# Optimization experiments

Hardware: AMD Instinct MI355X
Metric: run time of the kernel (lower is better)

Reference implementation:

```python
import jax, jax.numpy as jnp
import numpy as np

N_NODES = 50000
N_GRAPHS = 512
HID = 128
IN = 128
SLOPE = 0.2  # LeakyReLU negative slope (PyG default)


def _gatv2(x, src, dst, Wl, bl, Wr, br, att, bias, n):
    # PyG GATv2Conv, 1 head: xl used for source/messages, xr for targets
    xl = x @ Wl + bl          # [N, H]
    xr = x @ Wr + br          # [N, H]
    # per-edge score: att . LeakyReLU(xl[j] + xr[i])
    e = jax.nn.leaky_relu(xl[src] + xr[dst], SLOPE) @ att  # [E]
    # softmax grouped by destination node (self loops guarantee nonempty groups)
    m = jax.ops.segment_max(e, dst, num_segments=n)
    p = jnp.exp(e - m[dst])
    s = jax.ops.segment_sum(p, dst, num_segments=n)
    alpha = p / s[dst]                                      # [E]
    out = jax.ops.segment_sum(alpha[:, None] * xl[src], dst, num_segments=n)
    return out + bias


def setup_inputs() -> dict:
    key = jax.random.key(0)
    ks = jax.random.split(key, 24)
    x = jax.random.normal(ks[0], (N_NODES, IN), jnp.float32)
    edge_index = jax.random.randint(ks[1], (2, 1600000), 0, N_NODES, jnp.int64)
    batch = jnp.sort(jax.random.randint(ks[2], (N_NODES,), 0, N_GRAPHS, jnp.int64))

    def lin(k, fi, fo):
        k1, k2 = jax.random.split(k)
        sc = 1.0 / np.sqrt(fi)
        return (jax.random.uniform(k1, (fi, fo), jnp.float32, -sc, sc),
                jax.random.uniform(k2, (fo,), jnp.float32, -sc, sc))

    d = {"x": x, "edge_index": edge_index, "batch": batch}
    dims = [(IN, HID), (HID, HID), (HID, HID)]
    for i, (fi, fo) in enumerate(dims, 1):
        Wl, bl = lin(ks[3 * i], fi, fo)
        Wr, br = lin(ks[3 * i + 1], fi, fo)
        d[f"Wl{i}"], d[f"bl{i}"] = Wl, bl
        d[f"Wr{i}"], d[f"br{i}"] = Wr, br
        d[f"att{i}"] = jax.random.normal(ks[3 * i + 2], (fo,), jnp.float32) / np.sqrt(fo)
        d[f"bias{i}"] = jnp.zeros((fo,), jnp.float32)
    d["W4"], d["b4"] = lin(ks[15], HID, 128)
    d["W5"], d["b5"] = lin(ks[16], 128, 64)
    d["W6"], d["b6"] = lin(ks[17], 64, 2)
    return d


def reference(x, edge_index, batch,
              Wl1, bl1, Wr1, br1, att1, bias1,
              Wl2, bl2, Wr2, br2, att2, bias2,
              Wl3, bl3, Wr3, br3, att3, bias3,
              W4, b4, W5, b5, W6, b6):
    n = x.shape[0]
    loop = jnp.arange(n, dtype=edge_index.dtype)
    src = jnp.concatenate([edge_index[0], loop])  # add_self_loops=True
    dst = jnp.concatenate([edge_index[1], loop])

    h = jax.nn.relu(_gatv2(x, src, dst, Wl1, bl1, Wr1, br1, att1, bias1, n))
    h = jax.nn.relu(_gatv2(h, src, dst, Wl2, bl2, Wr2, br2, att2, bias2, n))
    h = _gatv2(h, src, dst, Wl3, bl3, Wr3, br3, att3, bias3, n)

    # global_mean_pool over graph ids
    sums = jax.ops.segment_sum(h, batch, num_segments=N_GRAPHS)
    cnts = jax.ops.segment_sum(jnp.ones((n,), h.dtype), batch, num_segments=N_GRAPHS)
    g = sums / jnp.maximum(cnts, 1.0)[:, None]

    # dropout is identity in eval mode; MLP head
    g = jax.nn.sigmoid(g @ W4 + b4)
    g = jax.nn.sigmoid(g @ W5 + b5)
    return g @ W6 + b6
```

## Files before the change

### kernel.cpp

```cpp
#include <hip/hip_runtime.h>
#include <hip/hip_bf16.h>
#include <math.h>

#define BK_SHIFT 7
#define BK_NODES 128

typedef _Float16 h2 __attribute__((ext_vector_type(2)));

__device__ __forceinline__ h2 u2h(unsigned u){ return __builtin_bit_cast(h2, u); }

__device__ __forceinline__ int dev_lower_bound(const int* __restrict__ a, int n, int v){
  int lo = 0, hi = n;
  while (lo < hi){ int mid = (lo + hi) >> 1; if (a[mid] < v) lo = mid + 1; else hi = mid; }
  return lo;
}

__global__ __launch_bounds__(256) void p1_bucket_count(const int* __restrict__ edst,
    int* __restrict__ bktTotal, int nE, int K){
  __shared__ int cnt[512];
  for (int k = threadIdx.x; k < K; k += 256) cnt[k] = 0;
  __syncthreads();
  int i = (blockIdx.x * 256 + threadIdx.x) * 8;
  if (i + 7 < nE){
    int4 a = *(const int4*)(edst + i);
    int4 b = *(const int4*)(edst + i + 4);
    atomicAdd(&cnt[a.x >> BK_SHIFT], 1); atomicAdd(&cnt[a.y >> BK_SHIFT], 1);
    atomicAdd(&cnt[a.z >> BK_SHIFT], 1); atomicAdd(&cnt[a.w >> BK_SHIFT], 1);
    atomicAdd(&cnt[b.x >> BK_SHIFT], 1); atomicAdd(&cnt[b.y >> BK_SHIFT], 1);
    atomicAdd(&cnt[b.z >> BK_SHIFT], 1); atomicAdd(&cnt[b.w >> BK_SHIFT], 1);
  } else {
    for (int j = i; j < nE; ++j) atomicAdd(&cnt[edst[j] >> BK_SHIFT], 1);
  }
  __syncthreads();
  for (int k = threadIdx.x; k < K; k += 256)
    if (cnt[k]) atomicAdd(&bktTotal[k], cnt[k]);
}

__global__ __launch_bounds__(512) void p2_scan(const int* __restrict__ bktTotal,
    int* __restrict__ bktBase, int* __restrict__ bktCur,
    int* __restrict__ row_off, int K, int n, int nE){
  __shared__ int sh[512];
  int t = threadIdx.x;
  int v = (t < K) ? bktTotal[t] : 0;
  sh[t] = v;
  __syncthreads();
  for (int off = 1; off < 512; off <<= 1){
    int u = (t >= off) ? sh[t - off] : 0;
    __syncthreads();
    sh[t] += u;
    __syncthreads();
  }
  if (t < K){
    int excl = sh[t] - v;
    bktBase[t] = excl;
    bktCur[t]  = excl;
  }
  if (t == 0){
    bktBase[K] = nE;
    row_off[n] = nE + n;
  }
}

__global__ __launch_bounds__(256) void p3_partition(const int* __restrict__ esrc,
    const int* __restrict__ edst, int* __restrict__ bktCur,
    int2* __restrict__ ebuf, int nE, int K){
  __shared__ int cnt[512];
  __shared__ int base[512];
  for (int k = threadIdx.x; k < K; k += 256) cnt[k] = 0;
  __syncthreads();
  const int i0 = (blockIdx.x * 256 + threadIdx.x) * 8;
  const int i1 = min(i0 + 8, nE);
  int bkt[8];
  int sv[8], dv[8];
  int cnt_local = i1 - i0;
  for (int j = 0; j < cnt_local; ++j){
    sv[j] = esrc[i0 + j];
    dv[j] = edst[i0 + j];
    bkt[j] = dv[j] >> BK_SHIFT;
    atomicAdd(&cnt[bkt[j]], 1);
  }
  __syncthreads();
  for (int k = threadIdx.x; k < K; k += 256){
    int c = cnt[k];
    base[k] = c ? atomicAdd(&bktCur[k], c) : 0;
  }
  __syncthreads();
  for (int k = threadIdx.x; k < K; k += 256) cnt[k] = 0;
  __syncthreads();
  for (int j = 0; j < cnt_local; ++j){
    int r = atomicAdd(&cnt[bkt[j]], 1);
    ebuf[base[bkt[j]] + r] = make_int2(sv[j], dv[j]);
  }
}

__global__ __launch_bounds__(256) void p4_build(const int2* __restrict__ ebuf,
    const int* __restrict__ bktBase, int* __restrict__ row_off,
    int* __restrict__ csr_src, int n){
  const int b = blockIdx.x;
  const int node0 = b << BK_SHIFT;
  const int nNodes = min(BK_NODES, n - node0);
  const int tid = threadIdx.x;
  __shared__ int ldeg[BK_NODES];
  __shared__ int lcur[BK_NODES];
  __shared__ int sc[BK_NODES];
  const int e0 = bktBase[b];
  const int e1 = bktBase[b + 1];
  if (tid < BK_NODES) ldeg[tid] = 0;
  __syncthreads();
  for (int i = e0 + tid; i < e1; i += 256)
    atomicAdd(&ldeg[ebuf[i].y - node0], 1);
  __syncthreads();
  if (tid < BK_NODES) sc[tid] = (tid < nNodes) ? (ldeg[tid] + 1) : 0;
  __syncthreads();
  for (int off = 1; off < BK_NODES; off <<= 1){
    int u = 0;
    if (tid < BK_NODES && tid >= off) u = sc[tid - off];
    __syncthreads();
    if (tid < BK_NODES) sc[tid] += u;
    __syncthreads();
  }
  if (tid < nNodes){
    const int csr0 = e0 + node0;
    int ro = csr0 + sc[tid] - (ldeg[tid] + 1);
    row_off[node0 + tid] = ro;
    lcur[tid] = ro;
  }
  __syncthreads();
  for (int i = e0 + tid; i < e1; i += 256){
    int2 e = ebuf[i];
    int p = atomicAdd(&lcur[e.y - node0], 1);
    csr_src[p] = e.x;
  }
  __syncthreads();
  if (tid < nNodes)
    csr_src[lcur[tid]] = node0 + tid;
}

__global__ __launch_bounds__(512) void gemm_xlxr_kernel(
    const float* __restrict__ X,
    const float* __restrict__ Wl, const float* __restrict__ bl,
    const float* __restrict__ Wr, const float* __restrict__ br,
    unsigned short* __restrict__ xl16, unsigned short* __restrict__ xr16, int n)
{
  const bool left = (blockIdx.y == 0);
  const float* W = left ? Wl : Wr;
  const float* b = left ? bl : br;
  unsigned short* o16 = left ? xl16 : xr16;
  __shared__ float Ws[32][128];
  __shared__ float Xs[128][36];
  const int tid = threadIdx.x;
  const int row0 = blockIdx.x * 128;
  const int tc = tid & 31;
  const int tr = tid >> 5;
  float acc[8][4] = {};
  for (int kc = 0; kc < 128; kc += 32){
    for (int idx = tid; idx < 1024; idx += 512){
      int r = idx >> 5, c4 = idx & 31;
      *(float4*)(&Ws[r][c4 * 4]) = *(const float4*)(W + (size_t)(kc + r) * 128 + c4 * 4);
    }
    for (int idx = tid; idx < 1024; idx += 512){
      int r = idx >> 3, c4 = idx & 7;
      int grow = row0 + r;
      float4 v = make_float4(0.f, 0.f, 0.f, 0.f);
      if (grow < n) v = *(const float4*)(X + (size_t)grow * 128 + kc + c4 * 4);
      *(float4*)(&Xs[r][c4 * 4]) = v;
    }
    __syncthreads();
    #pragma unroll
    for (int k = 0; k < 32; ++k){
      float4 w = *(const float4*)(&Ws[k][tc * 4]);
      #pragma unroll
      for (int r = 0; r < 8; ++r){
        float xv = Xs[tr * 8 + r][k];
        acc[r][0] = fmaf(xv, w.x, acc[r][0]);
        acc[r][1] = fmaf(xv, w.y, acc[r][1]);
        acc[r][2] = fmaf(xv, w.z, acc[r][2]);
        acc[r][3] = fmaf(xv, w.w, acc[r][3]);
      }
    }
    __syncthreads();
  }
  float4 bv = *(const float4*)(b + tc * 4);
  #pragma unroll
  for (int r = 0; r < 8; ++r){
    int grow = row0 + tr * 8 + r;
    if (grow < n){
      _Float16 h0 = (_Float16)(acc[r][0] + bv.x);
      _Float16 h1 = (_Float16)(acc[r][1] + bv.y);
      _Float16 h2v= (_Float16)(acc[r][2] + bv.z);
      _Float16 h3 = (_Float16)(acc[r][3] + bv.w);
      ushort4 o;
      o.x = __builtin_bit_cast(unsigned short, h0);
      o.y = __builtin_bit_cast(unsigned short, h1);
      o.z = __builtin_bit_cast(unsigned short, h2v);
      o.w = __builtin_bit_cast(unsigned short, h3);
      *(ushort4*)(o16 + (size_t)grow * 128 + tc * 4) = o;
    }
  }
}

__global__ __launch_bounds__(256) void edge_attn_kernel(
    const unsigned short* __restrict__ xl16, const unsigned short* __restrict__ xr16,
    const int* __restrict__ row_off, const int* __restrict__ csr_src,
    const float* __restrict__ att, const float* __restrict__ bias,
    float* __restrict__ out, int n, int do_relu)
{
  const int node = (blockIdx.x * blockDim.x + threadIdx.x) >> 4;
  const int nodec = min(node, n - 1);
  const int lane16 = threadIdx.x & 15;
  const int f8 = lane16 * 8;

  const uint4 xru = *(const uint4*)(xr16 + (size_t)nodec * 128 + f8);
  const h2 xr0 = u2h(xru.x), xr1 = u2h(xru.y), xr2 = u2h(xru.z), xr3 = u2h(xru.w);
  const float4 aA = *(const float4*)(att + f8);
  const float4 aB = *(const float4*)(att + f8 + 4);
  const h2 at0 = {(_Float16)aA.x, (_Float16)aA.y};
  const h2 at1 = {(_Float16)aA.z, (_Float16)aA.w};
  const h2 at2 = {(_Float16)aB.x, (_Float16)aB.y};
  const h2 at3 = {(_Float16)aB.z, (_Float16)aB.w};
  const h2 k02 = {(_Float16)0.2f, (_Float16)0.2f};

  const int base = row_off[nodec];
  const int deg  = row_off[nodec + 1] - base;
  int dmax = max(deg, __shfl_xor(deg, 16));
  dmax = max(dmax, __shfl_xor(dmax, 32));

  auto part = [&](uint4 xp) -> float {
    h2 u0 = u2h(xp.x) + xr0;
    h2 u1 = u2h(xp.y) + xr1;
    h2 u2 = u2h(xp.z) + xr2;
    h2 u3 = u2h(xp.w) + xr3;
    u0 = __builtin_elementwise_max(u0, u0 * k02);
    u1 = __builtin_elementwise_max(u1, u1 * k02);
    u2 = __builtin_elementwise_max(u2, u2 * k02);
    u3 = __builtin_elementwise_max(u3, u3 * k02);
    float ps = __builtin_amdgcn_fdot2(u0, at0, 0.f, false);
    ps = __builtin_amdgcn_fdot2(u1, at1, ps, false);
    ps = __builtin_amdgcn_fdot2(u2, at2, ps, false);
    ps = __builtin_amdgcn_fdot2(u3, at3, ps, false);
    return ps;
  };

  uint4 xp = *(const uint4*)(xl16 + (size_t)csr_src[base] * 128 + f8);
  float p = part(xp);
  p += __shfl_xor(p, 1); p += __shfl_xor(p, 2);
  p += __shfl_xor(p, 4); p += __shfl_xor(p, 8);
  float m = p, Mrun = p, s = 1.f;
  {
    h2 v0 = u2h(xp.x), v1 = u2h(xp.y), v2 = u2h(xp.z), v3 = u2h(xp.w);
    (void)v0;
  }
  float a0 = (float)u2h(xp.x).x, a1 = (float)u2h(xp.x).y;
  float a2 = (float)u2h(xp.y).x, a3 = (float)u2h(xp.y).y;
  float a4 = (float)u2h(xp.z).x, a5 = (float)u2h(xp.z).y;
  float a6 = (float)u2h(xp.w).x, a7 = (float)u2h(xp.w).y;

  for (int it = 1; it < dmax; it += 4){
    const int c0 = min(it,     deg - 1);
    const int c1 = min(it + 1, deg - 1);
    const int c2 = min(it + 2, deg - 1);
    const int c3 = min(it + 3, deg - 1);
    const int s0 = csr_src[base + c0];
    const int s1 = csr_src[base + c1];
    const int s2 = csr_src[base + c2];
    const int s3 = csr_src[base + c3];
    const uint4 xA = *(const uint4*)(xl16 + (size_t)s0 * 128 + f8);
    const uint4 xB = *(const uint4*)(xl16 + (size_t)s1 * 128 + f8);
    const uint4 xC = *(const uint4*)(xl16 + (size_t)s2 * 128 + f8);
    const uint4 xD = *(const uint4*)(xl16 + (size_t)s3 * 128 + f8);
    float pA = part(xA), pB = part(xB), pC = part(xC), pD = part(xD);
    #pragma unroll
    for (int off = 1; off < 16; off <<= 1){
      pA += __shfl_xor(pA, off);
      pB += __shfl_xor(pB, off);
      pC += __shfl_xor(pC, off);
      pD += __shfl_xor(pD, off);
    }
    const bool vA = it < deg, vB = it + 1 < deg, vC = it + 2 < deg, vD = it + 3 < deg;
    float fA = vA ? pA : -3.0e38f;
    float fB = vB ? pB : -3.0e38f;
    float fC = vC ? pC : -3.0e38f;
    float fD = vD ? pD : -3.0e38f;
    Mrun = fmaxf(Mrun, fmaxf(fmaxf(fA, fB), fmaxf(fC, fD)));
    if (__any(Mrun > m + 8.f)){
      float sc = __expf(m - Mrun);
      s *= sc;
      a0 *= sc; a1 *= sc; a2 *= sc; a3 *= sc;
      a4 *= sc; a5 *= sc; a6 *= sc; a7 *= sc;
      m = Mrun;
    }
    float qA = vA ? __expf(pA - m) : 0.f;
    float qB = vB ? __expf(pB - m) : 0.f;
    float qC = vC ? __expf(pC - m) : 0.f;
    float qD = vD ? __expf(pD - m) : 0.f;
    s += (qA + qB) + (qC + qD);
    h2 w;
    w = u2h(xA.x); a0 = fmaf(qA, (float)w.x, a0); a1 = fmaf(qA, (float)w.y, a1);
    w = u2h(xA.y); a2 = fmaf(qA, (float)w.x, a2); a3 = fmaf(qA, (float)w.y, a3);
    w = u2h(xA.z); a4 = fmaf(qA, (float)w.x, a4); a5 = fmaf(qA, (float)w.y, a5);
    w = u2h(xA.w); a6 = fmaf(qA, (float)w.x, a6); a7 = fmaf(qA, (float)w.y, a7);
    w = u2h(xB.x); a0 = fmaf(qB, (float)w.x, a0); a1 = fmaf(qB, (float)w.y, a1);
    w = u2h(xB.y); a2 = fmaf(qB, (float)w.x, a2); a3 = fmaf(qB, (float)w.y, a3);
    w = u2h(xB.z); a4 = fmaf(qB, (float)w.x, a4); a5 = fmaf(qB, (float)w.y, a5);
    w = u2h(xB.w); a6 = fmaf(qB, (float)w.x, a6); a7 = fmaf(qB, (float)w.y, a7);
    w = u2h(xC.x); a0 = fmaf(qC, (float)w.x, a0); a1 = fmaf(qC, (float)w.y, a1);
    w = u2h(xC.y); a2 = fmaf(qC, (float)w.x, a2); a3 = fmaf(qC, (float)w.y, a3);
    w = u2h(xC.z); a4 = fmaf(qC, (float)w.x, a4); a5 = fmaf(qC, (float)w.y, a5);
    w = u2h(xC.w); a6 = fmaf(qC, (float)w.x, a6); a7 = fmaf(qC, (float)w.y, a7);
    w = u2h(xD.x); a0 = fmaf(qD, (float)w.x, a0); a1 = fmaf(qD, (float)w.y, a1);
    w = u2h(xD.y); a2 = fmaf(qD, (float)w.x, a2); a3 = fmaf(qD, (float)w.y, a3);
    w = u2h(xD.z); a4 = fmaf(qD, (float)w.x, a4); a5 = fmaf(qD, (float)w.y, a5);
    w = u2h(xD.w); a6 = fmaf(qD, (float)w.x, a6); a7 = fmaf(qD, (float)w.y, a7);
  }

  if (node < n){
    const float inv = 1.0f / s;
    const float4 bA = *(const float4*)(bias + f8);
    const float4 bB = *(const float4*)(bias + f8 + 4);
    float o0 = fmaf(a0, inv, bA.x), o1 = fmaf(a1, inv, bA.y);
    float o2 = fmaf(a2, inv, bA.z), o3 = fmaf(a3, inv, bA.w);
    float o4 = fmaf(a4, inv, bB.x), o5 = fmaf(a5, inv, bB.y);
    float o6 = fmaf(a6, inv, bB.z), o7 = fmaf(a7, inv, bB.w);
    if (do_relu){
      o0 = fmaxf(o0, 0.f); o1 = fmaxf(o1, 0.f); o2 = fmaxf(o2, 0.f); o3 = fmaxf(o3, 0.f);
      o4 = fmaxf(o4, 0.f); o5 = fmaxf(o5, 0.f); o6 = fmaxf(o6, 0.f); o7 = fmaxf(o7, 0.f);
    }
    *(float4*)(out + (size_t)node * 128 + f8)     = make_float4(o0, o1, o2, o3);
    *(float4*)(out + (size_t)node * 128 + f8 + 4) = make_float4(o4, o5, o6, o7);
  }
}

__global__ __launch_bounds__(128) void pool_mlp_kernel(
    const float* __restrict__ h, const int* __restrict__ batch, int n,
    const float* __restrict__ W4, const float* __restrict__ b4,
    const float* __restrict__ W5, const float* __restrict__ b5,
    const float* __restrict__ W6, const float* __restrict__ b6,
    float* __restrict__ out)
{
  int g = blockIdx.x;
  int t = threadIdx.x;
  __shared__ float gf[128];
  __shared__ float h1[128];
  __shared__ float h2s[64];
  int lo = dev_lower_bound(batch, n, g);
  int hi = dev_lower_bound(batch, n, g + 1);
  float ssum = 0.f;
  for (int i = lo; i < hi; ++i) ssum += h[(size_t)i * 128 + t];
  float cnt = (float)(hi - lo);
  gf[t] = ssum / fmaxf(cnt, 1.0f);
  __syncthreads();
  float a = b4[t];
  for (int k = 0; k < 128; ++k) a = fmaf(gf[k], W4[k * 128 + t], a);
  h1[t] = 1.0f / (1.0f + __expf(-a));
  __syncthreads();
  if (t < 64){
    float a5 = b5[t];
    for (int k = 0; k < 128; ++k) a5 = fmaf(h1[k], W5[k * 64 + t], a5);
    h2s[t] = 1.0f / (1.0f + __expf(-a5));
  }
  __syncthreads();
  if (t < 2){
    float a6 = b6[t];
    for (int k = 0; k < 64; ++k) a6 = fmaf(h2s[k], W6[k * 2 + t], a6);
    out[g * 2 + t] = a6;
  }
}

extern "C" void kernel_launch(void* const* d_in, const int* in_sizes, int n_in,
                              void* d_out, int out_size, void* d_ws, size_t ws_size,
                              hipStream_t stream)
{
  const float* x          = (const float*)d_in[0];
  const int*   edge_index = (const int*)d_in[1];
  const int*   batch      = (const int*)d_in[2];
  const int n  = in_sizes[0] / 128;
  const int nE = in_sizes[1] / 2;
  const int* esrc = edge_index;
  const int* edst = edge_index + nE;
  const int n_graphs = out_size / 2;
  const int K = (n + BK_NODES - 1) >> BK_SHIFT;

  const float *Wl[3], *bl[3], *Wr[3], *br[3], *att[3], *bias[3];
  for (int l = 0; l < 3; ++l){
    Wl[l]   = (const float*)d_in[3 + 6 * l + 0];
    bl[l]   = (const float*)d_in[3 + 6 * l + 1];
    Wr[l]   = (const float*)d_in[3 + 6 * l + 2];
    br[l]   = (const float*)d_in[3 + 6 * l + 3];
    att[l]  = (const float*)d_in[3 + 6 * l + 4];
    bias[l] = (const float*)d_in[3 + 6 * l + 5];
  }
  const float* W4 = (const float*)d_in[21]; const float* b4 = (const float*)d_in[22];
  const float* W5 = (const float*)d_in[23]; const float* b5 = (const float*)d_in[24];
  const float* W6 = (const float*)d_in[25]; const float* b6 = (const float*)d_in[26];

  char* ws = (char*)d_ws;
  size_t off = 0;
  auto alloc = [&](size_t bytes) -> void* {
    void* p = ws + off;
    off = (off + bytes + 255) & ~(size_t)255;
    return p;
  };
  int*   row_off  = (int*)  alloc((size_t)(n + 1) * sizeof(int));
  int*   bktTotal = (int*)  alloc(512 * sizeof(int));
  int*   bktBase  = (int*)  alloc(513 * sizeof(int));
  int*   bktCur   = (int*)  alloc(512 * sizeof(int));
  int*   csr_src  = (int*)  alloc((size_t)(nE + n) * sizeof(int));
  int2*  ebuf     = (int2*) alloc((size_t)nE * sizeof(int2));
  unsigned short* xlb16 = (unsigned short*)alloc((size_t)n * 128 * sizeof(unsigned short));
  unsigned short* xrb16 = (unsigned short*)alloc((size_t)n * 128 * sizeof(unsigned short));
  float* hC       = (float*)alloc((size_t)n * 128 * sizeof(float));
  (void)ws_size; (void)n_in;

  hipMemsetAsync(bktTotal, 0, 512 * sizeof(int), stream);
  const int eblocks = (nE + 2048 - 1) / 2048;
  p1_bucket_count<<<eblocks, 256, 0, stream>>>(edst, bktTotal, nE, K);
  p2_scan<<<1, 512, 0, stream>>>(bktTotal, bktBase, bktCur, row_off, K, n, nE);
  p3_partition<<<eblocks, 256, 0, stream>>>(esrc, edst, bktCur, ebuf, nE, K);
  p4_build<<<K, 256, 0, stream>>>(ebuf, bktBase, row_off, csr_src, n);

  const int gemm_tiles = (n + 127) / 128;
  const int attn_blocks = (int)(((size_t)n * 16 + 255) / 256);

  gemm_xlxr_kernel<<<dim3(gemm_tiles, 2), 512, 0, stream>>>(x, Wl[0], bl[0], Wr[0], br[0],
                                                            xlb16, xrb16, n);
  edge_attn_kernel<<<attn_blocks, 256, 0, stream>>>(xlb16, xrb16, row_off, csr_src,
                                                    att[0], bias[0], hC, n, 1);
  gemm_xlxr_kernel<<<dim3(gemm_tiles, 2), 512, 0, stream>>>(hC, Wl[1], bl[1], Wr[1], br[1],
                                                            xlb16, xrb16, n);
  edge_attn_kernel<<<attn_blocks, 256, 0, stream>>>(xlb16, xrb16, row_off, csr_src,
                                                    att[1], bias[1], hC, n, 1);
  gemm_xlxr_kernel<<<dim3(gemm_tiles, 2), 512, 0, stream>>>(hC, Wl[2], bl[2], Wr[2], br[2],
                                                            xlb16, xrb16, n);
  edge_attn_kernel<<<attn_blocks, 256, 0, stream>>>(xlb16, xrb16, row_off, csr_src,
                                                    att[2], bias[2], hC, n, 0);

  pool_mlp_kernel<<<n_graphs, 128, 0, stream>>>(hC, batch, n, W4, b4, W5, b5, W6, b6,
                                                (float*)d_out);
}
```

Measured before the change: 458.4 us.

## Replace FP32 SIMT projection GEMM with FP16 MFMA kernel using pre-transposed weights

```diff
diff --git a/kernel.cpp b/kernel.cpp
--- a/kernel.cpp
+++ b/kernel.cpp
@@ -6,6 +6,8 @@
 #define BK_NODES 128
 
 typedef _Float16 h2 __attribute__((ext_vector_type(2)));
+typedef _Float16 f16x8 __attribute__((ext_vector_type(8)));
+typedef float f32x4 __attribute__((ext_vector_type(4)));
 
 __device__ __forceinline__ h2 u2h(unsigned u){ return __builtin_bit_cast(h2, u); }
 
@@ -136,65 +138,91 @@
     csr_src[lcur[tid]] = node0 + tid;
 }
 
-__global__ __launch_bounds__(512) void gemm_xlxr_kernel(
+__global__ __launch_bounds__(256) void prep_w_kernel(
+    const float* __restrict__ W0, const float* __restrict__ W1,
+    const float* __restrict__ W2, const float* __restrict__ W3,
+    const float* __restrict__ W4m, const float* __restrict__ W5m,
+    unsigned short* __restrict__ Wt16)
+{
+  const float* Ws[6] = {W0, W1, W2, W3, W4m, W5m};
+  const int mat = blockIdx.x >> 3;
+  const int chunk = blockIdx.x & 7;
+  const float* W = Ws[mat];
+  unsigned short* o = Wt16 + mat * 16384;
+  #pragma unroll
+  for (int e = 0; e < 8; ++e){
+    int i = chunk * 2048 + e * 256 + threadIdx.x;
+    int k = i >> 7, col = i & 127;
+    _Float16 h = (_Float16)W[i];
+    o[col * 128 + k] = __builtin_bit_cast(unsigned short, h);
+  }
+}
+
+__global__ __launch_bounds__(256) void gemm_mfma_kernel(
     const float* __restrict__ X,
-    const float* __restrict__ Wl, const float* __restrict__ bl,
-    const float* __restrict__ Wr, const float* __restrict__ br,
+    const unsigned short* __restrict__ WtL,
+    const float* __restrict__ bl, const float* __restrict__ br,
     unsigned short* __restrict__ xl16, unsigned short* __restrict__ xr16, int n)
 {
-  const bool left = (blockIdx.y == 0);
-  const float* W = left ? Wl : Wr;
-  const float* b = left ? bl : br;
-  unsigned short* o16 = left ? xl16 : xr16;
-  __shared__ float Ws[32][128];
-  __shared__ float Xs[128][36];
-  const int tid = threadIdx.x;
-  const int row0 = blockIdx.x * 128;
-  const int tc = tid & 31;
-  const int tr = tid >> 5;
-  float acc[8][4] = {};
-  for (int kc = 0; kc < 128; kc += 32){
-    for (int idx = tid; idx < 1024; idx += 512){
-      int r = idx >> 5, c4 = idx & 31;
-      *(float4*)(&Ws[r][c4 * 4]) = *(const float4*)(W + (size_t)(kc + r) * 128 + c4 * 4);
-    }
-    for (int idx = tid; idx < 1024; idx += 512){
-      int r = idx >> 3, c4 = idx & 7;
-      int grow = row0 + r;
-      float4 v = make_float4(0.f, 0.f, 0.f, 0.f);
-      if (grow < n) v = *(const float4*)(X + (size_t)grow * 128 + kc + c4 * 4);
-      *(float4*)(&Xs[r][c4 * 4]) = v;
-    }
-    __syncthreads();
+  const int mat = blockIdx.y;
+  const unsigned short* Wt = WtL + mat * 16384;
+  const float* bias = mat ? br : bl;
+  unsigned short* out = mat ? xr16 : xl16;
+  const int w   = threadIdx.x >> 6;
+  const int l   = threadIdx.x & 63;
+  const int l15 = l & 15;
+  const int kq  = l >> 4;
+  const int rowbase = blockIdx.x * 128 + w * 32;
+
+  f16x8 a[2][4];
+  #pragma unroll
+  for (int rt = 0; rt < 2; ++rt){
+    const int r = rowbase + rt * 16 + l15;
+    const bool ok = r < n;
+    const float* src = X + (size_t)min(r, n - 1) * 128 + kq * 8;
     #pragma unroll
-    for (int k = 0; k < 32; ++k){
-      float4 w = *(const float4*)(&Ws[k][tc * 4]);
+    for (int ks = 0; ks < 4; ++ks){
+      float4 f0 = ok ? *(const float4*)(src + ks * 32)     : make_float4(0.f,0.f,0.f,0.f);
+      float4 f1 = ok ? *(const float4*)(src + ks * 32 + 4) : make_float4(0.f,0.f,0.f,0.f);
+      f16x8 v;
+      v[0] = (_Float16)f0.x; v[1] = (_Float16)f0.y;
+      v[2] = (_Float16)f0.z; v[3] = (_Float16)f0.w;
+      v[4] = (_Float16)f1.x; v[5] = (_Float16)f1.y;
+      v[6] = (_Float16)f1.z; v[7] = (_Float16)f1.w;
+      a[rt][ks] = v;
+    }
+  }
+
+  f32x4 acc[2][8];
+  #pragma unroll
+  for (int rt = 0; rt < 2; ++rt)
+    #pragma unroll
+    for (int ct = 0; ct < 8; ++ct)
+      acc[rt][ct] = (f32x4){0.f, 0.f, 0.f, 0.f};
+
+  #pragma unroll
+  for (int ks = 0; ks < 4; ++ks){
+    #pragma unroll
+    for (int ct = 0; ct < 8; ++ct){
+      f16x8 b = *(const f16x8*)(Wt + (size_t)(ct * 16 + l15) * 128 + ks * 32 + kq * 8);
+      acc[0][ct] = __builtin_amdgcn_mfma_f32_16x16x32_f16(a[0][ks], b, acc[0][ct], 0, 0, 0);
+      acc[1][ct] = __builtin_amdgcn_mfma_f32_16x16x32_f16(a[1][ks], b, acc[1][ct], 0, 0, 0);
+    }
+  }
+
+  #pragma unroll
+  for (int ct = 0; ct < 8; ++ct){
+    const float bv = bias[ct * 16 + l15];
+    #pragma unroll
+    for (int rt = 0; rt < 2; ++rt){
       #pragma unroll
-      for (int r = 0; r < 8; ++r){
-        float xv = Xs[tr * 8 + r][k];
-        acc[r][0] = fmaf(xv, w.x, acc[r][0]);
-        acc[r][1] = fmaf(xv, w.y, acc[r][1]);
-        acc[r][2] = fmaf(xv, w.z, acc[r][2]);
-        acc[r][3] = fmaf(xv, w.w, acc[r][3]);
+      for (int rg = 0; rg < 4; ++rg){
+        const int r = rowbase + rt * 16 + kq * 4 + rg;
+        if (r < n){
+          _Float16 h = (_Float16)(acc[rt][ct][rg] + bv);
+          out[(size_t)r * 128 + ct * 16 + l15] = __builtin_bit_cast(unsigned short, h);
+        }
       }
-    }
-    __syncthreads();
-  }
-  float4 bv = *(const float4*)(b + tc * 4);
-  #pragma unroll
-  for (int r = 0; r < 8; ++r){
-    int grow = row0 + tr * 8 + r;
-    if (grow < n){
-      _Float16 h0 = (_Float16)(acc[r][0] + bv.x);
-      _Float16 h1 = (_Float16)(acc[r][1] + bv.y);
-      _Float16 h2v= (_Float16)(acc[r][2] + bv.z);
-      _Float16 h3 = (_Float16)(acc[r][3] + bv.w);
-      ushort4 o;
-      o.x = __builtin_bit_cast(unsigned short, h0);
-      o.y = __builtin_bit_cast(unsigned short, h1);
-      o.z = __builtin_bit_cast(unsigned short, h2v);
-      o.w = __builtin_bit_cast(unsigned short, h3);
-      *(ushort4*)(o16 + (size_t)grow * 128 + tc * 4) = o;
     }
   }
 }
@@ -246,10 +274,6 @@
   p += __shfl_xor(p, 1); p += __shfl_xor(p, 2);
   p += __shfl_xor(p, 4); p += __shfl_xor(p, 8);
   float m = p, Mrun = p, s = 1.f;
-  {
-    h2 v0 = u2h(xp.x), v1 = u2h(xp.y), v2 = u2h(xp.z), v3 = u2h(xp.w);
-    (void)v0;
-  }
   float a0 = (float)u2h(xp.x).x, a1 = (float)u2h(xp.x).y;
   float a2 = (float)u2h(xp.y).x, a3 = (float)u2h(xp.y).y;
   float a4 = (float)u2h(xp.z).x, a5 = (float)u2h(xp.z).y;
@@ -408,8 +432,11 @@
   int2*  ebuf     = (int2*) alloc((size_t)nE * sizeof(int2));
   unsigned short* xlb16 = (unsigned short*)alloc((size_t)n * 128 * sizeof(unsigned short));
   unsigned short* xrb16 = (unsigned short*)alloc((size_t)n * 128 * sizeof(unsigned short));
+  unsigned short* Wt16  = (unsigned short*)alloc(6 * 16384 * sizeof(unsigned short));
   float* hC       = (float*)alloc((size_t)n * 128 * sizeof(float));
   (void)ws_size; (void)n_in;
+
+  prep_w_kernel<<<48, 256, 0, stream>>>(Wl[0], Wr[0], Wl[1], Wr[1], Wl[2], Wr[2], Wt16);
 
   hipMemsetAsync(bktTotal, 0, 512 * sizeof(int), stream);
   const int eblocks = (nE + 2048 - 1) / 2048;
@@ -421,16 +448,16 @@
   const int gemm_tiles = (n + 127) / 128;
   const int attn_blocks = (int)(((size_t)n * 16 + 255) / 256);
 
-  gemm_xlxr_kernel<<<dim3(gemm_tiles, 2), 512, 0, stream>>>(x, Wl[0], bl[0], Wr[0], br[0],
-                                                            xlb16, xrb16, n);
+  gemm_mfma_kernel<<<dim3(gemm_tiles, 2), 256, 0, stream>>>(x, Wt16 + 0 * 32768,
+                                                            bl[0], br[0], xlb16, xrb16, n);
   edge_attn_kernel<<<attn_blocks, 256, 0, stream>>>(xlb16, xrb16, row_off, csr_src,
                                                     att[0], bias[0], hC, n, 1);
-  gemm_xlxr_kernel<<<dim3(gemm_tiles, 2), 512, 0, stream>>>(hC, Wl[1], bl[1], Wr[1], br[1],
-                                                            xlb16, xrb16, n);
+  gemm_mfma_kernel<<<dim3(gemm_tiles, 2), 256, 0, stream>>>(hC, Wt16 + 1 * 32768,
+                                                            bl[1], br[1], xlb16, xrb16, n);
   edge_attn_kernel<<<attn_blocks, 256, 0, stream>>>(xlb16, xrb16, row_off, csr_src,
                                                     att[1], bias[1], hC, n, 1);
-  gemm_xlxr_kernel<<<dim3(gemm_tiles, 2), 512, 0, stream>>>(hC, Wl[2], bl[2], Wr[2], br[2],
-                                                            xlb16, xrb16, n);
+  gemm_mfma_kernel<<<dim3(gemm_tiles, 2), 256, 0, stream>>>(hC, Wt16 + 2 * 32768,
+                                                            bl[2], br[2], xlb16, xrb16, n);
   edge_attn_kernel<<<attn_blocks, 256, 0, stream>>>(xlb16, xrb16, row_off, csr_src,
                                                     att[2], bias[2], hC, n, 0);
 
```

Result: faster. 435.3 us (-5.0%).
